# Performance work log

Measured on AMD Instinct MI355X. Metric: run time of the kernel, lower is better.

## Reference

```python
import jax, jax.numpy as jnp
import numpy as np

_EPS_COS = 1e-8  # F.cosine_similarity default eps
_EPS_ADD = 1e-12


def setup_inputs() -> dict:
    key = jax.random.key(0)
    ks = jax.random.split(key, 7)
    B, N, M, INT_SHIFT = 256, 4096, 64, 3
    return {
        "beta": jax.random.uniform(ks[0], (B, 1), dtype=jnp.float32),
        "kappa": jax.random.normal(ks[1], (B, M), dtype=jnp.float32),
        "gamma": jax.random.uniform(ks[2], (B, 1), dtype=jnp.float32),
        "g": jax.random.uniform(ks[3], (B, 1), dtype=jnp.float32),
        "s": jax.random.uniform(ks[4], (B, INT_SHIFT), dtype=jnp.float32),
        "w_prev": jax.random.uniform(ks[5], (B, N), dtype=jnp.float32),
        "memory": jax.random.normal(ks[6], (B, N, M), dtype=jnp.float32),
        "int_shift": INT_SHIFT,
    }


def reference(beta, kappa, gamma, g, s, w_prev, memory, int_shift):
    # --- content addressing: cosine similarity + softmax over N ---
    a = memory + _EPS_ADD                      # [B, N, M]
    b = kappa[:, None, :] + _EPS_ADD           # [B, 1, M]
    dot = jnp.einsum("bnm,bqm->bn", a, b)
    na = jnp.sqrt(jnp.sum(a * a, axis=-1))     # [B, N]
    nb = jnp.sqrt(jnp.sum(b * b, axis=-1))     # [B, 1]
    sim = dot / (jnp.maximum(na, _EPS_COS) * jnp.maximum(nb, _EPS_COS))
    w_c = jax.nn.softmax(beta * sim, axis=1)   # [B, N]

    # --- interpolate with previous weighting ---
    w_g = g * w_c + (1.0 - g) * w_prev         # [B, N]

    # --- circular shift: result[b, i] = sum_j s[b, j] * w_g[b, (i + j - 1) mod N]
    # (equivalent to the per-batch padded conv1d in the original, batched via roll)
    w_hat = jnp.zeros_like(w_g)
    for j in range(int_shift):
        w_hat = w_hat + s[:, j:j + 1] * jnp.roll(w_g, 1 - j, axis=1)

    # --- sharpen ---
    w = w_hat ** gamma
    w = w / (jnp.sum(w, axis=1, keepdims=True) + _EPS_ADD)
    return w
```

## Files before the change

### kernel.cpp

```cpp
#include <hip/hip_runtime.h>
#include <math.h>

#define EPS_COS 1e-8f
#define EPS_ADD 1e-12f


constexpr int NTHREADS = 1024;
constexpr int NWAVES   = NTHREADS / 64;
constexpr int MAX_N    = 4096;

__global__ __launch_bounds__(NTHREADS, 1) void ntm_attention_kernel(
    const float* __restrict__ beta,
    const float* __restrict__ kappa,
    const float* __restrict__ gamma,
    const float* __restrict__ g,
    const float* __restrict__ s,
    const float* __restrict__ w_prev,
    const float* __restrict__ mem,
    float* __restrict__ out,
    int N, int S)
{
    const int b    = blockIdx.x;
    const int tid  = threadIdx.x;
    const int lane = tid & 63;
    const int wave = tid >> 6;
    const int l16  = lane & 15;
    const int rgrp = lane >> 4;

    __shared__ float t_sh[MAX_N];
    __shared__ float w_sh[MAX_N];
    __shared__ float red[NWAVES];

    float4 kv = *reinterpret_cast<const float4*>(kappa + (size_t)b * 64 + l16 * 4);
    kv.x += EPS_ADD; kv.y += EPS_ADD; kv.z += EPS_ADD; kv.w += EPS_ADD;

    float nb2 = kv.x * kv.x + kv.y * kv.y + kv.z * kv.z + kv.w * kv.w;
#pragma unroll
    for (int m = 1; m < 16; m <<= 1) nb2 += __shfl_xor(nb2, m);
    const float nb = fmaxf(sqrtf(nb2), EPS_COS);
    const float bv = beta[b];

    const size_t base = (size_t)b * N * 64;
    float tmax = -INFINITY;

    const int nIter = N / 64;
    for (int it = 0; it < nIter; it += 4) {
        const int row0 = it * 64 + wave * 4 + rgrp;
        const float4* p = reinterpret_cast<const float4*>(mem + base + (size_t)row0 * 64) + l16;
        float4 a0 = p[0];
        float4 a1 = p[1024];
        float4 a2 = p[2048];
        float4 a3 = p[3072];

#pragma unroll
        for (int k = 0; k < 4; ++k) {
            float4 a = (k == 0) ? a0 : (k == 1) ? a1 : (k == 2) ? a2 : a3;
            a.x += EPS_ADD; a.y += EPS_ADD; a.z += EPS_ADD; a.w += EPS_ADD;
            float d  = a.x * kv.x + a.y * kv.y + a.z * kv.z + a.w * kv.w;
            float n2 = a.x * a.x + a.y * a.y + a.z * a.z + a.w * a.w;
#pragma unroll
            for (int m = 1; m < 16; m <<= 1) {
                d  += __shfl_xor(d, m);
                n2 += __shfl_xor(n2, m);
            }
            const float na = fmaxf(sqrtf(n2), EPS_COS);
            const float t  = bv * (d / (na * nb));
            const int row  = row0 + k * 64;
            if (l16 == 0) t_sh[row] = t;
            tmax = fmaxf(tmax, t);
        }
    }

#pragma unroll
    for (int m = 1; m < 64; m <<= 1) tmax = fmaxf(tmax, __shfl_xor(tmax, m));
    if (lane == 0) red[wave] = tmax;
    __syncthreads();
    float gmax = red[0];
#pragma unroll
    for (int i = 1; i < NWAVES; ++i) gmax = fmaxf(gmax, red[i]);
    __syncthreads();

    float lsum = 0.0f;
    for (int i = tid; i < N; i += NTHREADS) {
        const float e = expf(t_sh[i] - gmax);
        t_sh[i] = e;
        lsum += e;
    }
#pragma unroll
    for (int m = 1; m < 64; m <<= 1) lsum += __shfl_xor(lsum, m);
    if (lane == 0) red[wave] = lsum;
    __syncthreads();
    float tot = 0.0f;
#pragma unroll
    for (int i = 0; i < NWAVES; ++i) tot += red[i];
    __syncthreads();

    const float gv = g[b];
    for (int i = tid; i < N; i += NTHREADS) {
        const float wc = t_sh[i] / tot;
        const float wp = w_prev[(size_t)b * N + i];
        w_sh[i] = gv * wc + (1.0f - gv) * wp;
    }
    __syncthreads();

    const float gam = gamma[b];
    float sv[8];
    const int Sc = (S < 8) ? S : 8;
    for (int j = 0; j < Sc; ++j) sv[j] = s[(size_t)b * S + j];

    float ssum = 0.0f;
    for (int i = tid; i < N; i += NTHREADS) {
        float wh = 0.0f;
        for (int j = 0; j < Sc; ++j) {
            int idx = i + j - 1;
            idx += N;
            if (idx >= N) idx -= N;
            if (idx >= N) idx -= N;
            wh += sv[j] * w_sh[idx];
        }
        const float sh = powf(wh, gam);
        t_sh[i] = sh;
        ssum += sh;
    }
#pragma unroll
    for (int m = 1; m < 64; m <<= 1) ssum += __shfl_xor(ssum, m);
    if (lane == 0) red[wave] = ssum;
    __syncthreads();
    float stot = 0.0f;
#pragma unroll
    for (int i = 0; i < NWAVES; ++i) stot += red[i];

    const float denom = stot + EPS_ADD;
    for (int i = tid; i < N; i += NTHREADS) {
        out[(size_t)b * N + i] = t_sh[i] / denom;
    }
}

extern "C" void kernel_launch(void* const* d_in, const int* in_sizes, int n_in,
                              void* d_out, int out_size, void* d_ws, size_t ws_size,
                              hipStream_t stream) {
    const float* beta   = (const float*)d_in[0];
    const float* kappa  = (const float*)d_in[1];
    const float* gamma  = (const float*)d_in[2];
    const float* g      = (const float*)d_in[3];
    const float* s      = (const float*)d_in[4];
    const float* w_prev = (const float*)d_in[5];
    const float* mem    = (const float*)d_in[6];
    float* out          = (float*)d_out;

    const int B = in_sizes[0];
    const int N = in_sizes[5] / B;
    const int S = in_sizes[4] / B;

    ntm_attention_kernel<<<B, NTHREADS, 0, stream>>>(
        beta, kappa, gamma, g, s, w_prev, mem, out, N, S);
}
```

Before: 54.20 us.

## Remap lanes to 4 per row, prefetch memory rows, stage w_prev in LDS

```diff
diff --git a/kernel.cpp b/kernel.cpp
--- a/kernel.cpp
+++ b/kernel.cpp
@@ -24,51 +24,72 @@
     const int tid  = threadIdx.x;
     const int lane = tid & 63;
     const int wave = tid >> 6;
-    const int l16  = lane & 15;
-    const int rgrp = lane >> 4;
+    const int q    = lane & 3;
+    const int r16  = lane >> 2;
 
     __shared__ float t_sh[MAX_N];
     __shared__ float w_sh[MAX_N];
+    __shared__ float wp_sh[MAX_N];
     __shared__ float red[NWAVES];
 
-    float4 kv = *reinterpret_cast<const float4*>(kappa + (size_t)b * 64 + l16 * 4);
-    kv.x += EPS_ADD; kv.y += EPS_ADD; kv.z += EPS_ADD; kv.w += EPS_ADD;
+    {
+        const float4* wp = reinterpret_cast<const float4*>(w_prev + (size_t)b * N);
+        float4* dst = reinterpret_cast<float4*>(wp_sh);
+        for (int i = tid; i < (N >> 2); i += NTHREADS) dst[i] = wp[i];
+    }
 
-    float nb2 = kv.x * kv.x + kv.y * kv.y + kv.z * kv.z + kv.w * kv.w;
+    float4 kv[4];
+    {
+        const float4* kp = reinterpret_cast<const float4*>(kappa + (size_t)b * 64);
 #pragma unroll
-    for (int m = 1; m < 16; m <<= 1) nb2 += __shfl_xor(nb2, m);
+        for (int j = 0; j < 4; ++j) {
+            kv[j] = kp[q + 4 * j];
+            kv[j].x += EPS_ADD; kv[j].y += EPS_ADD;
+            kv[j].z += EPS_ADD; kv[j].w += EPS_ADD;
+        }
+    }
+    float nb2 = 0.0f;
+#pragma unroll
+    for (int j = 0; j < 4; ++j)
+        nb2 += kv[j].x * kv[j].x + kv[j].y * kv[j].y + kv[j].z * kv[j].z + kv[j].w * kv[j].w;
+    nb2 += __shfl_xor(nb2, 1);
+    nb2 += __shfl_xor(nb2, 2);
     const float nb = fmaxf(sqrtf(nb2), EPS_COS);
-    const float bv = beta[b];
+    const float bv_over_nb = beta[b] / nb;
 
-    const size_t base = (size_t)b * N * 64;
+    const float4* mp = reinterpret_cast<const float4*>(mem + (size_t)b * N * 64);
+    const int nIter = N >> 8;
     float tmax = -INFINITY;
 
-    const int nIter = N / 64;
-    for (int it = 0; it < nIter; it += 4) {
-        const int row0 = it * 64 + wave * 4 + rgrp;
-        const float4* p = reinterpret_cast<const float4*>(mem + base + (size_t)row0 * 64) + l16;
-        float4 a0 = p[0];
-        float4 a1 = p[1024];
-        float4 a2 = p[2048];
-        float4 a3 = p[3072];
+    int row0 = wave * 16 + r16;
+    const float4* p = mp + (size_t)row0 * 16 + q;
+    float4 a0 = p[0], a1 = p[4], a2 = p[8], a3 = p[12];
 
-#pragma unroll
-        for (int k = 0; k < 4; ++k) {
-            float4 a = (k == 0) ? a0 : (k == 1) ? a1 : (k == 2) ? a2 : a3;
-            a.x += EPS_ADD; a.y += EPS_ADD; a.z += EPS_ADD; a.w += EPS_ADD;
-            float d  = a.x * kv.x + a.y * kv.y + a.z * kv.z + a.w * kv.w;
-            float n2 = a.x * a.x + a.y * a.y + a.z * a.z + a.w * a.w;
-#pragma unroll
-            for (int m = 1; m < 16; m <<= 1) {
-                d  += __shfl_xor(d, m);
-                n2 += __shfl_xor(n2, m);
-            }
-            const float na = fmaxf(sqrtf(n2), EPS_COS);
-            const float t  = bv * (d / (na * nb));
-            const int row  = row0 + k * 64;
-            if (l16 == 0) t_sh[row] = t;
-            tmax = fmaxf(tmax, t);
+    for (int it = 0; it < nIter; ++it) {
+        const float4 c0 = a0, c1 = a1, c2 = a2, c3 = a3;
+        if (it + 1 < nIter) {
+            const float4* pn = p + (size_t)(it + 1) * 4096;
+            a0 = pn[0]; a1 = pn[4]; a2 = pn[8]; a3 = pn[12];
         }
+
+        float d = 0.0f, n2 = 0.0f;
+        d += c0.x * kv[0].x + c0.y * kv[0].y + c0.z * kv[0].z + c0.w * kv[0].w;
+        d += c1.x * kv[1].x + c1.y * kv[1].y + c1.z * kv[1].z + c1.w * kv[1].w;
+        d += c2.x * kv[2].x + c2.y * kv[2].y + c2.z * kv[2].z + c2.w * kv[2].w;
+        d += c3.x * kv[3].x + c3.y * kv[3].y + c3.z * kv[3].z + c3.w * kv[3].w;
+        n2 += c0.x * c0.x + c0.y * c0.y + c0.z * c0.z + c0.w * c0.w;
+        n2 += c1.x * c1.x + c1.y * c1.y + c1.z * c1.z + c1.w * c1.w;
+        n2 += c2.x * c2.x + c2.y * c2.y + c2.z * c2.z + c2.w * c2.w;
+        n2 += c3.x * c3.x + c3.y * c3.y + c3.z * c3.z + c3.w * c3.w;
+
+        d  += __shfl_xor(d, 1);  d  += __shfl_xor(d, 2);
+        n2 += __shfl_xor(n2, 1); n2 += __shfl_xor(n2, 2);
+
+        const float inv_na = rsqrtf(fmaxf(n2, 1e-16f));
+        const float t = bv_over_nb * d * inv_na;
+        const int row = row0 + it * 256;
+        if (q == 0) t_sh[row] = t;
+        tmax = fmaxf(tmax, t);
     }
 
 #pragma unroll
@@ -96,10 +117,10 @@
     __syncthreads();
 
     const float gv = g[b];
+    const float inv_tot = 1.0f / tot;
     for (int i = tid; i < N; i += NTHREADS) {
-        const float wc = t_sh[i] / tot;
-        const float wp = w_prev[(size_t)b * N + i];
-        w_sh[i] = gv * wc + (1.0f - gv) * wp;
+        const float wc = t_sh[i] * inv_tot;
+        w_sh[i] = gv * wc + (1.0f - gv) * wp_sh[i];
     }
     __syncthreads();
 
@@ -112,8 +133,7 @@
     for (int i = tid; i < N; i += NTHREADS) {
         float wh = 0.0f;
         for (int j = 0; j < Sc; ++j) {
-            int idx = i + j - 1;
-            idx += N;
+            int idx = i + j - 1 + N;
             if (idx >= N) idx -= N;
             if (idx >= N) idx -= N;
             wh += sv[j] * w_sh[idx];
@@ -130,9 +150,9 @@
 #pragma unroll
     for (int i = 0; i < NWAVES; ++i) stot += red[i];
 
-    const float denom = stot + EPS_ADD;
+    const float inv_den = 1.0f / (stot + EPS_ADD);
     for (int i = tid; i < N; i += NTHREADS) {
-        out[(size_t)b * N + i] = t_sh[i] / denom;
+        out[(size_t)b * N + i] = t_sh[i] * inv_den;
     }
 }
 
```

After: 56.86 us. 4.9% more time.

## Split scores into a many-block streaming kernel and a per-row softmax/shift tail kernel

Applied to the files above, without the earlier changes.

```diff
diff --git a/kernel.cpp b/kernel.cpp
--- a/kernel.cpp
+++ b/kernel.cpp
@@ -4,19 +4,75 @@
 #define EPS_COS 1e-8f
 #define EPS_ADD 1e-12f
 
+typedef float f4 __attribute__((ext_vector_type(4)));
 
-constexpr int NTHREADS = 1024;
-constexpr int NWAVES   = NTHREADS / 64;
-constexpr int MAX_N    = 4096;
-
-__global__ __launch_bounds__(NTHREADS, 1) void ntm_attention_kernel(
+__global__ __launch_bounds__(256) void ntm_scores_kernel(
     const float* __restrict__ beta,
     const float* __restrict__ kappa,
+    const float* __restrict__ mem,
+    float* __restrict__ t_out,
+    int N, int chunks)
+{
+    const int blk  = blockIdx.x;
+    const int b    = blk / chunks;
+    const int c    = blk % chunks;
+    const int tid  = threadIdx.x;
+    const int lane = tid & 63;
+    const int wave = tid >> 6;
+    const int l16  = lane & 15;
+    const int rg   = lane >> 4;
+    const int r_off = wave * 4 + rg;
+
+    f4 kv = *reinterpret_cast<const f4*>(kappa + (size_t)b * 64 + l16 * 4);
+    kv += (f4)EPS_ADD;
+    float nb2 = kv.x * kv.x + kv.y * kv.y + kv.z * kv.z + kv.w * kv.w;
+#pragma unroll
+    for (int m = 1; m < 16; m <<= 1) nb2 += __shfl_xor(nb2, m);
+    const float bscale = beta[b] / fmaxf(sqrtf(nb2), EPS_COS);
+
+    const int row_base = c * 256;
+    const f4* p = reinterpret_cast<const f4*>(mem) +
+                  ((size_t)b * N + row_base + r_off) * 16 + l16;
+    f4 a[4];
+#pragma unroll
+    for (int u = 0; u < 4; ++u) a[u] = __builtin_nontemporal_load(p + u * 256);
+
+    const size_t obase = (size_t)b * N + row_base + r_off;
+
+    for (int r0 = 0; r0 < 16; r0 += 4) {
+        f4 cb[4];
+#pragma unroll
+        for (int u = 0; u < 4; ++u) cb[u] = a[u];
+        if (r0 + 4 < 16) {
+#pragma unroll
+            for (int u = 0; u < 4; ++u)
+                a[u] = __builtin_nontemporal_load(p + (size_t)(r0 + 4 + u) * 256);
+        }
+#pragma unroll
+        for (int u = 0; u < 4; ++u) {
+            const f4 v = cb[u];
+            float d  = v.x * kv.x + v.y * kv.y + v.z * kv.z + v.w * kv.w;
+            float n2 = v.x * v.x + v.y * v.y + v.z * v.z + v.w * v.w;
+#pragma unroll
+            for (int m = 1; m < 16; m <<= 1) {
+                d  += __shfl_xor(d, m);
+                n2 += __shfl_xor(n2, m);
+            }
+            const float t = bscale * d * rsqrtf(fmaxf(n2, 1e-16f));
+            if (l16 == 0) t_out[obase + (r0 + u) * 16] = t;
+        }
+    }
+}
+
+constexpr int NT2    = 1024;
+constexpr int NW2    = NT2 / 64;
+constexpr int MAX_N  = 4096;
+
+__global__ __launch_bounds__(NT2, 1) void ntm_tail_kernel(
     const float* __restrict__ gamma,
     const float* __restrict__ g,
     const float* __restrict__ s,
     const float* __restrict__ w_prev,
-    const float* __restrict__ mem,
     float* __restrict__ out,
     int N, int S)
 {
@@ -24,64 +80,30 @@
     const int tid  = threadIdx.x;
     const int lane = tid & 63;
     const int wave = tid >> 6;
-    const int l16  = lane & 15;
-    const int rgrp = lane >> 4;
 
     __shared__ float t_sh[MAX_N];
     __shared__ float w_sh[MAX_N];
-    __shared__ float red[NWAVES];
+    __shared__ float red[NW2];
 
-    float4 kv = *reinterpret_cast<const float4*>(kappa + (size_t)b * 64 + l16 * 4);
-    kv.x += EPS_ADD; kv.y += EPS_ADD; kv.z += EPS_ADD; kv.w += EPS_ADD;
+    float* tb = out + (size_t)b * N;
 
-    float nb2 = kv.x * kv.x + kv.y * kv.y + kv.z * kv.z + kv.w * kv.w;
-#pragma unroll
-    for (int m = 1; m < 16; m <<= 1) nb2 += __shfl_xor(nb2, m);
-    const float nb = fmaxf(sqrtf(nb2), EPS_COS);
-    const float bv = beta[b];
-
-    const size_t base = (size_t)b * N * 64;
     float tmax = -INFINITY;
-
-    const int nIter = N / 64;
-    for (int it = 0; it < nIter; it += 4) {
-        const int row0 = it * 64 + wave * 4 + rgrp;
-        const float4* p = reinterpret_cast<const float4*>(mem + base + (size_t)row0 * 64) + l16;
-        float4 a0 = p[0];
-        float4 a1 = p[1024];
-        float4 a2 = p[2048];
-        float4 a3 = p[3072];
-
-#pragma unroll
-        for (int k = 0; k < 4; ++k) {
-            float4 a = (k == 0) ? a0 : (k == 1) ? a1 : (k == 2) ? a2 : a3;
-            a.x += EPS_ADD; a.y += EPS_ADD; a.z += EPS_ADD; a.w += EPS_ADD;
-            float d  = a.x * kv.x + a.y * kv.y + a.z * kv.z + a.w * kv.w;
-            float n2 = a.x * a.x + a.y * a.y + a.z * a.z + a.w * a.w;
-#pragma unroll
-            for (int m = 1; m < 16; m <<= 1) {
-                d  += __shfl_xor(d, m);
-                n2 += __shfl_xor(n2, m);
-            }
-            const float na = fmaxf(sqrtf(n2), EPS_COS);
-            const float t  = bv * (d / (na * nb));
-            const int row  = row0 + k * 64;
-            if (l16 == 0) t_sh[row] = t;
-            tmax = fmaxf(tmax, t);
-        }
+    for (int i = tid; i < N; i += NT2) {
+        const float v = tb[i];
+        t_sh[i] = v;
+        tmax = fmaxf(tmax, v);
     }
-
 #pragma unroll
     for (int m = 1; m < 64; m <<= 1) tmax = fmaxf(tmax, __shfl_xor(tmax, m));
     if (lane == 0) red[wave] = tmax;
     __syncthreads();
     float gmax = red[0];
 #pragma unroll
-    for (int i = 1; i < NWAVES; ++i) gmax = fmaxf(gmax, red[i]);
+    for (int i = 1; i < NW2; ++i) gmax = fmaxf(gmax, red[i]);
     __syncthreads();
 
     float lsum = 0.0f;
-    for (int i = tid; i < N; i += NTHREADS) {
+    for (int i = tid; i < N; i += NT2) {
         const float e = expf(t_sh[i] - gmax);
         t_sh[i] = e;
         lsum += e;
@@ -92,14 +114,14 @@
     __syncthreads();
     float tot = 0.0f;
 #pragma unroll
-    for (int i = 0; i < NWAVES; ++i) tot += red[i];
+    for (int i = 0; i < NW2; ++i) tot += red[i];
     __syncthreads();
 
     const float gv = g[b];
-    for (int i = tid; i < N; i += NTHREADS) {
-        const float wc = t_sh[i] / tot;
-        const float wp = w_prev[(size_t)b * N + i];
-        w_sh[i] = gv * wc + (1.0f - gv) * wp;
+    const float inv_tot = 1.0f / tot;
+    for (int i = tid; i < N; i += NT2) {
+        const float wc = t_sh[i] * inv_tot;
+        w_sh[i] = gv * wc + (1.0f - gv) * w_prev[(size_t)b * N + i];
     }
     __syncthreads();
 
@@ -109,11 +131,10 @@
     for (int j = 0; j < Sc; ++j) sv[j] = s[(size_t)b * S + j];
 
     float ssum = 0.0f;
-    for (int i = tid; i < N; i += NTHREADS) {
+    for (int i = tid; i < N; i += NT2) {
         float wh = 0.0f;
         for (int j = 0; j < Sc; ++j) {
-            int idx = i + j - 1;
-            idx += N;
+            int idx = i + j - 1 + N;
             if (idx >= N) idx -= N;
             if (idx >= N) idx -= N;
             wh += sv[j] * w_sh[idx];
@@ -128,11 +149,11 @@
     __syncthreads();
     float stot = 0.0f;
 #pragma unroll
-    for (int i = 0; i < NWAVES; ++i) stot += red[i];
+    for (int i = 0; i < NW2; ++i) stot += red[i];
 
-    const float denom = stot + EPS_ADD;
-    for (int i = tid; i < N; i += NTHREADS) {
-        out[(size_t)b * N + i] = t_sh[i] / denom;
+    const float inv_den = 1.0f / (stot + EPS_ADD);
+    for (int i = tid; i < N; i += NT2) {
+        tb[i] = t_sh[i] * inv_den;
     }
 }
 
@@ -151,7 +172,10 @@
     const int B = in_sizes[0];
     const int N = in_sizes[5] / B;
     const int S = in_sizes[4] / B;
+    const int chunks = N / 256;
 
-    ntm_attention_kernel<<<B, NTHREADS, 0, stream>>>(
-        beta, kappa, gamma, g, s, w_prev, mem, out, N, S);
+    ntm_scores_kernel<<<B * chunks, 256, 0, stream>>>(
+        beta, kappa, mem, out, N, chunks);
+    ntm_tail_kernel<<<B, NT2, 0, stream>>>(
+        gamma, g, s, w_prev, out, N, S);
 }
```

Result: slower. 62.22 us (+14.8%).
